# Performance work log

Hardware: AMD Instinct MI355X
Metric: run time of the kernel (lower is better)

The kernel has to match this reference:

```python
import jax, jax.numpy as jnp
import numpy as np

N = 100000   # nodes
E = 1600000  # edges
D = 128      # input_dim == hidden_dim
L = 3        # num_layers
G = 256      # graphs in batch
EPS = 1e-5   # BatchNorm eps


def setup_inputs() -> dict:
    key = jax.random.key(0)
    ks = jax.random.split(key, 10)
    x = jax.random.normal(ks[0], (N, D), dtype=jnp.float32)
    edge_index = jax.random.randint(ks[1], (2, E), 0, N, dtype=jnp.int64)
    batch = jnp.sort(jax.random.randint(ks[2], (N,), 0, G, dtype=jnp.int64))
    # stacked per-layer params (all layers are D->D since input_dim==hidden_dim)
    W = jax.random.normal(ks[3], (L, D, D), dtype=jnp.float32) * 0.05
    b = jax.random.normal(ks[4], (L, D), dtype=jnp.float32) * 0.02
    gamma = 1.0 + 0.1 * jax.random.normal(ks[5], (L, D), dtype=jnp.float32)
    beta = 0.1 * jax.random.normal(ks[6], (L, D), dtype=jnp.float32)
    rmean = 0.05 * jax.random.normal(ks[7], (L, D), dtype=jnp.float32)
    rvar = jax.random.uniform(ks[8], (L, D), minval=0.5, maxval=1.5, dtype=jnp.float32)
    return {"x": x, "W": W, "b": b, "gamma": gamma, "beta": beta,
            "rmean": rmean, "rvar": rvar, "edge_index": edge_index, "batch": batch}


def reference(x, W, b, gamma, beta, rmean, rvar, edge_index, batch):
    # --- GCN normalization with self-loops (same for every layer) ---
    src, dst = edge_index[0], edge_index[1]
    loop = jnp.arange(N, dtype=src.dtype)
    s = jnp.concatenate([src, loop])  # [E+N]
    d = jnp.concatenate([dst, loop])
    deg = jax.ops.segment_sum(jnp.ones(E + N, x.dtype), d, num_segments=N)
    dinv = jnp.where(deg > 0, jax.lax.rsqrt(deg), 0.0)
    norm = dinv[s] * dinv[d]  # [E+N]

    h = x
    for i in range(L):
        m = h @ W[i]                                            # [N, D] dense GEMM
        agg = jax.ops.segment_sum(m[s] * norm[:, None], d, num_segments=N)
        h = agg + b[i]
        # BatchNorm1d (inference: running stats), then ReLU; dropout is identity in eval
        h = (h - rmean[i]) * jax.lax.rsqrt(rvar[i] + EPS) * gamma[i] + beta[i]
        h = jax.nn.relu(h)

    # --- global mean / max pooling by graph id ---
    counts = jax.ops.segment_sum(jnp.ones(N, h.dtype), batch, num_segments=G)
    mean_pool = jax.ops.segment_sum(h, batch, num_segments=G) / jnp.maximum(counts, 1.0)[:, None]
    max_pool = jax.ops.segment_max(h, batch, num_segments=G)
    return jnp.concatenate([mean_pool, max_pool], axis=1)  # [G, 2D]
```

## Files before the change

kernel.cpp:

```cpp
#include <hip/hip_runtime.h>
#include <math.h>
#include <float.h>

#define D 128

typedef short short8 __attribute__((ext_vector_type(8)));
typedef float f32x4 __attribute__((ext_vector_type(4)));

__device__ __forceinline__ unsigned int bf16r(float f) {
    unsigned int u = __float_as_uint(f);
    return (u + 0x7fffu + ((u >> 16) & 1u)) >> 16;
}
__device__ __forceinline__ float bf2f(unsigned int lo16) {
    return __uint_as_float(lo16 << 16);
}

#define GBM0 64
__global__ __launch_bounds__(256) void prep_fused(
    const int* __restrict__ dst, int* __restrict__ cnt, int* __restrict__ rank, int E,
    const float* __restrict__ x, unsigned short* __restrict__ mraw, int n,
    const float* __restrict__ W, const float* __restrict__ b,
    const float* __restrict__ gamma, const float* __restrict__ beta,
    const float* __restrict__ rmean, const float* __restrict__ rvar,
    unsigned short* __restrict__ Wt, float* __restrict__ sc, float* __restrict__ sh, int L_,
    const int* __restrict__ batch, int* __restrict__ gstart, int G,
    int cb, int gb, int wb) {
    __shared__ short Wl[D * 136];
    const int blk = blockIdx.x;
    const int tid = threadIdx.x;
    if (blk < cb) {
        int base = (blk * 256 + tid) * 4;
        if (base + 4 <= E) {
            int4 d = *(const int4*)&dst[base];
            int r0 = atomicAdd(&cnt[d.x], 1);
            int r1 = atomicAdd(&cnt[d.y], 1);
            int r2 = atomicAdd(&cnt[d.z], 1);
            int r3 = atomicAdd(&cnt[d.w], 1);
            *(int4*)&rank[base] = make_int4(r0, r1, r2, r3);
        } else if (base < E) {
            for (int e = base; e < E; ++e) rank[e] = atomicAdd(&cnt[dst[e]], 1);
        }
    } else if (blk < cb + gb) {
#pragma unroll
        for (int i = 0; i < 64; ++i) {
            int t = i * 256 + tid;
            int k = t >> 7, r = t & 127;
            Wl[r * 136 + k] = (short)bf16r(W[t]);
        }
        __syncthreads();

        const int row0 = (blk - cb) * GBM0;
        const int wid = tid >> 6;
        const int lane = tid & 63;
        const int lr = lane & 15;
        const int lg = lane >> 4;
        const int grow = row0 + wid * 16 + lr;
        const bool valid = grow < n;

        f32x4 acc[8];
#pragma unroll
        for (int fc = 0; fc < 8; ++fc) acc[fc] = (f32x4){0.f, 0.f, 0.f, 0.f};

#pragma unroll
        for (int ks = 0; ks < 4; ++ks) {
            int kb = ks * 32 + lg * 8;
            float4 va = make_float4(0.f, 0.f, 0.f, 0.f);
            float4 vb = make_float4(0.f, 0.f, 0.f, 0.f);
            if (valid) {
                va = *(const float4*)&x[(size_t)grow * D + kb];
                vb = *(const float4*)&x[(size_t)grow * D + kb + 4];
            }
            uint4 pk;
            pk.x = bf16r(va.x) | (bf16r(va.y) << 16);
            pk.y = bf16r(va.z) | (bf16r(va.w) << 16);
            pk.z = bf16r(vb.x) | (bf16r(vb.y) << 16);
            pk.w = bf16r(vb.z) | (bf16r(vb.w) << 16);
            short8 y = *(short8*)&pk;
#pragma unroll
            for (int fc = 0; fc < 8; ++fc) {
                short8 xf = *(const short8*)&Wl[(fc * 16 + lr) * 136 + kb];
                acc[fc] = __builtin_amdgcn_mfma_f32_16x16x32_bf16(xf, y, acc[fc], 0, 0, 0);
            }
        }

        if (valid) {
#pragma unroll
            for (int fc = 0; fc < 8; ++fc) {
                int gcol = fc * 16 + lg * 4;
                uint2 pk;
                pk.x = bf16r(acc[fc][0]) | (bf16r(acc[fc][1]) << 16);
                pk.y = bf16r(acc[fc][2]) | (bf16r(acc[fc][3]) << 16);
                *(uint2*)&mraw[(size_t)grow * D + gcol] = pk;
            }
        }
    } else if (blk < cb + gb + wb) {
        int t = (blk - cb - gb) * 256 + tid;
        int total = L_ * D * D;
        if (t < total) {
            int l = t / (D * D), rem = t % (D * D);
            int r = rem >> 7, k = rem & 127;
            Wt[t] = (unsigned short)bf16r(W[l * D * D + k * D + r]);
        }
        if (t < L_ * D) {
            float inv = rsqrtf(rvar[t] + 1e-5f);
            float s = inv * gamma[t];
            sc[t] = s;
            sh[t] = (b[t] - rmean[t]) * s + beta[t];
        }
    } else {
        int i = (blk - cb - gb - wb) * 256 + tid;
        if (i >= n) return;
        int g = batch[i];
        int gp = (i == 0) ? -1 : batch[i - 1];
        for (int gg = gp + 1; gg <= g; ++gg) gstart[gg] = i;
        if (i == n - 1) for (int gg = g + 1; gg <= G; ++gg) gstart[gg] = n;
    }
}


__global__ void scan1(const int* __restrict__ cnt, int* __restrict__ rp, int* __restrict__ aux,
                      float* __restrict__ dinv, int n) {
    __shared__ int sh[256];
    int tid = threadIdx.x;
    int base = blockIdx.x * 1024 + tid * 4;
    int v[4]; int s = 0;
#pragma unroll
    for (int i = 0; i < 4; i++) {
        int idx = base + i;
        int t = (idx < n) ? cnt[idx] : 0;
        if (idx < n) dinv[idx] = rsqrtf((float)t + 1.0f);
        v[i] = s; s += t;
    }
    sh[tid] = s; __syncthreads();
    for (int off = 1; off < 256; off <<= 1) {
        int t = (tid >= off) ? sh[tid - off] : 0;
        __syncthreads();
        sh[tid] += t;
        __syncthreads();
    }
    int excl = sh[tid] - s;
#pragma unroll
    for (int i = 0; i < 4; i++) { int idx = base + i; if (idx < n) rp[idx] = excl + v[i]; }
    if (tid == 255) aux[blockIdx.x] = sh[255];
}

__global__ void scan2(int* aux, int nb) {
    __shared__ int sh[256];
    int tid = threadIdx.x;
    int v = (tid < nb) ? aux[tid] : 0;
    sh[tid] = v; __syncthreads();
    for (int off = 1; off < 256; off <<= 1) {
        int t = (tid >= off) ? sh[tid - off] : 0;
        __syncthreads();
        sh[tid] += t;
        __syncthreads();
    }
    if (tid < nb) aux[tid] = sh[tid] - v;
}

__global__ __launch_bounds__(256) void fill_scale(
    const int* __restrict__ src, const int* __restrict__ dst,
    const int* __restrict__ rp, const int* __restrict__ aux,
    const int* __restrict__ rank, int* __restrict__ csr, int E,
    unsigned int* __restrict__ M, const float* __restrict__ dinv, int n,
    int fb) {
    const int blk = blockIdx.x;
    const int tid = threadIdx.x;
    if (blk < fb) {
        int base = (blk * 256 + tid) * 4;
        if (base + 4 <= E) {
            int4 d = *(const int4*)&dst[base];
            int4 s = *(const int4*)&src[base];
            int4 r = *(const int4*)&rank[base];
            int p0 = rp[d.x] + aux[d.x >> 10];
            int p1 = rp[d.y] + aux[d.y >> 10];
            int p2 = rp[d.z] + aux[d.z >> 10];
            int p3 = rp[d.w] + aux[d.w >> 10];
            csr[p0 + r.x] = s.x;
            csr[p1 + r.y] = s.y;
            csr[p2 + r.z] = s.z;
            csr[p3 + r.w] = s.w;
        } else if (base < E) {
            for (int e = base; e < E; ++e)
                csr[rp[dst[e]] + aux[dst[e] >> 10] + rank[e]] = src[e];
        }
    } else {
        int t = (blk - fb) * 256 + tid;
        int total4 = n * 16;
        if (t >= total4) return;
        int row = t >> 4;
        float di = dinv[row];
        uint4 v = *(uint4*)&M[(size_t)t * 4];
        uint4 o;
        o.x = bf16r(bf2f(v.x & 0xffffu) * di) | (bf16r(bf2f(v.x >> 16) * di) << 16);
        o.y = bf16r(bf2f(v.y & 0xffffu) * di) | (bf16r(bf2f(v.y >> 16) * di) << 16);
        o.z = bf16r(bf2f(v.z & 0xffffu) * di) | (bf16r(bf2f(v.z >> 16) * di) << 16);
        o.w = bf16r(bf2f(v.w & 0xffffu) * di) | (bf16r(bf2f(v.w >> 16) * di) << 16);
        *(uint4*)&M[(size_t)t * 4] = o;
    }
}

#define GBM 128
__global__ __launch_bounds__(512) void gemm_mfma(const unsigned short* __restrict__ hin,
                                                 const unsigned short* __restrict__ Wt,
                                                 const float* __restrict__ dinv,
                                                 unsigned short* __restrict__ mout, int n) {
    __shared__ short Ah[GBM * 136];
    __shared__ short Wl[D * 136];
    const int tid = threadIdx.x;
    const int row0 = blockIdx.x * GBM;

#pragma unroll
    for (int i = 0; i < 4; ++i) {
        int c = tid + i * 512;
        int r = c >> 4, ck = (c & 15) * 8;
        int grow = row0 + r;
        int4 v = make_int4(0, 0, 0, 0);
        if (grow < n) v = *(const int4*)&hin[(size_t)grow * D + ck];
        *(int4*)&Ah[r * 136 + ck] = v;
    }
#pragma unroll
    for (int i = 0; i < 4; ++i) {
        int c = tid + i * 512;
        int r = c >> 4, ck = (c & 15) * 8;
        *(int4*)&Wl[r * 136 + ck] = *(const int4*)&Wt[(size_t)r * D + ck];
    }
    __syncthreads();

    const int wid = tid >> 6;
    const int lane = tid & 63;
    const int lr = lane & 15;
    const int lg = lane >> 4;

    f32x4 acc[8];
#pragma unroll
    for (int fc = 0; fc < 8; ++fc) acc[fc] = (f32x4){0.f, 0.f, 0.f, 0.f};

#pragma unroll
    for (int ks = 0; ks < 4; ++ks) {
        int kb = ks * 32 + lg * 8;
        short8 y = *(const short8*)&Ah[(wid * 16 + lr) * 136 + kb];
#pragma unroll
        for (int fc = 0; fc < 8; ++fc) {
            short8 xf = *(const short8*)&Wl[(fc * 16 + lr) * 136 + kb];
            acc[fc] = __builtin_amdgcn_mfma_f32_16x16x32_bf16(xf, y, acc[fc], 0, 0, 0);
        }
    }

    int grow = row0 + wid * 16 + lr;
    if (grow < n) {
        float di = dinv[grow];
#pragma unroll
        for (int fc = 0; fc < 8; ++fc) {
            int gcol = fc * 16 + lg * 4;
            uint2 pk;
            pk.x = bf16r(acc[fc][0] * di) | (bf16r(acc[fc][1] * di) << 16);
            pk.y = bf16r(acc[fc][2] * di) | (bf16r(acc[fc][3] * di) << 16);
            *(uint2*)&mout[(size_t)grow * D + gcol] = pk;
        }
    }
}

__global__ __launch_bounds__(256) void agg_bf16(const unsigned int* __restrict__ M,
                                                const int* __restrict__ rp,
                                                const int* __restrict__ aux,
                                                const int* __restrict__ csr,
                                                const float* __restrict__ dinv,
                                                const float* __restrict__ sc,
                                                const float* __restrict__ sh,
                                                unsigned int* __restrict__ H, int n, int Etot) {
    const int wid = threadIdx.x >> 6;
    const int lane = threadIdx.x & 63;
    const int row = blockIdx.x * 4 + wid;
    if (row >= n) return;

    unsigned int u = M[(unsigned)row * 64u + lane];
    float a0 = bf2f(u & 0xffffu);
    float a1 = bf2f(u >> 16);

    int e = rp[row] + aux[row >> 10];
    const int end = (row + 1 < n) ? rp[row + 1] + aux[(row + 1) >> 10] : Etot;
    const int n16 = (end - e) >> 4;

    if (n16 > 0) {
        int sa[16];
#pragma unroll
        for (int i = 0; i < 16; ++i) sa[i] = csr[e + i];
        for (int it = 0; it < n16; ++it) {
            int sb[16];
            if (it + 1 < n16) {
#pragma unroll
                for (int i = 0; i < 16; ++i) sb[i] = csr[e + 16 + i];
            } else {
#pragma unroll
                for (int i = 0; i < 16; ++i) sb[i] = 0;
            }
            unsigned int g[16];
#pragma unroll
            for (int i = 0; i < 16; ++i) g[i] = M[(unsigned)sa[i] * 64u + lane];
#pragma unroll
            for (int i = 0; i < 16; ++i) {
                a0 += bf2f(g[i] & 0xffffu);
                a1 += bf2f(g[i] >> 16);
            }
#pragma unroll
            for (int i = 0; i < 16; ++i) sa[i] = sb[i];
            e += 16;
        }
    }
    for (; e + 4 <= end; e += 4) {
        int s[4];
#pragma unroll
        for (int i = 0; i < 4; ++i) s[i] = csr[e + i];
        unsigned int g[4];
#pragma unroll
        for (int i = 0; i < 4; ++i) g[i] = M[(unsigned)s[i] * 64u + lane];
#pragma unroll
        for (int i = 0; i < 4; ++i) {
            a0 += bf2f(g[i] & 0xffffu);
            a1 += bf2f(g[i] >> 16);
        }
    }
    for (; e < end; ++e) {
        unsigned int gs = M[(unsigned)csr[e] * 64u + lane];
        a0 += bf2f(gs & 0xffffu);
        a1 += bf2f(gs >> 16);
    }

    float di = dinv[row];
    int c0 = lane * 2;
    float v0 = fmaxf(a0 * di * sc[c0] + sh[c0], 0.f);
    float v1 = fmaxf(a1 * di * sc[c0 + 1] + sh[c0 + 1], 0.f);
    H[(unsigned)row * 64u + lane] = bf16r(v0) | (bf16r(v1) << 16);
}

__global__ __launch_bounds__(64) void pool1(const unsigned int* __restrict__ H,
                                            const int* __restrict__ gstart,
                                            float4* __restrict__ pbuf) {
    int g = blockIdx.x, c = blockIdx.y;
    int lane = threadIdx.x;
    int beg = gstart[g], end = gstart[g + 1];
    int len = end - beg;
    int cb = beg + (int)(((long long)len * c) >> 3);
    int ce = beg + (int)(((long long)len * (c + 1)) >> 3);
    float s0 = 0.f, s1 = 0.f, m0 = -INFINITY, m1 = -INFINITY;
    int i = cb;
    for (; i + 2 <= ce; i += 2) {
        unsigned int ua = H[(size_t)i * 64 + lane];
        unsigned int ub = H[(size_t)(i + 1) * 64 + lane];
        float a0 = bf2f(ua & 0xffffu), a1 = bf2f(ua >> 16);
        float b0 = bf2f(ub & 0xffffu), b1 = bf2f(ub >> 16);
        s0 += a0 + b0; s1 += a1 + b1;
        m0 = fmaxf(m0, fmaxf(a0, b0)); m1 = fmaxf(m1, fmaxf(a1, b1));
    }
    for (; i < ce; ++i) {
        unsigned int ua = H[(size_t)i * 64 + lane];
        float a0 = bf2f(ua & 0xffffu), a1 = bf2f(ua >> 16);
        s0 += a0; s1 += a1;
        m0 = fmaxf(m0, a0); m1 = fmaxf(m1, a1);
    }
    pbuf[((size_t)g * 8 + c) * 64 + lane] = make_float4(s0, s1, m0, m1);
}

__global__ __launch_bounds__(64) void pool2(const float4* __restrict__ pbuf,
                                            const int* __restrict__ gstart,
                                            float* __restrict__ out) {
    int g = blockIdx.x;
    int lane = threadIdx.x;
    float s0 = 0.f, s1 = 0.f, m0 = -INFINITY, m1 = -INFINITY;
#pragma unroll
    for (int c = 0; c < 8; ++c) {
        float4 p = pbuf[((size_t)g * 8 + c) * 64 + lane];
        s0 += p.x; s1 += p.y;
        m0 = fmaxf(m0, p.z); m1 = fmaxf(m1, p.w);
    }
    float cnt = fmaxf((float)(gstart[g + 1] - gstart[g]), 1.0f);
    int c0 = lane * 2;
    out[g * (2 * D) + c0] = s0 / cnt;
    out[g * (2 * D) + c0 + 1] = s1 / cnt;
    out[g * (2 * D) + D + c0] = m0;
    out[g * (2 * D) + D + c0 + 1] = m1;
}

extern "C" void kernel_launch(void* const* d_in, const int* in_sizes, int n_in,
                              void* d_out, int out_size, void* d_ws, size_t ws_size,
                              hipStream_t stream) {
    const float* x     = (const float*)d_in[0];
    const float* W     = (const float*)d_in[1];
    const float* b     = (const float*)d_in[2];
    const float* gamma = (const float*)d_in[3];
    const float* beta  = (const float*)d_in[4];
    const float* rmean = (const float*)d_in[5];
    const float* rvar  = (const float*)d_in[6];
    const int*   eidx  = (const int*)d_in[7];
    const int*   batch = (const int*)d_in[8];

    const int N = in_sizes[8];
    const int E = in_sizes[7] / 2;
    const int L = in_sizes[2] / D;
    const int G = out_size / (2 * D);

    const int* esrc = eidx;
    const int* edst = eidx + E;

    size_t off = 0;
    auto carve = [&](size_t bytes) { size_t cur = off; off += (bytes + 255) & ~(size_t)255; return cur; };
    char* base = (char*)d_ws;
    const int nb = (N + 1023) / 1024;

    int*            cnt  = (int*)           (base + carve((size_t)N * 4));
    int*            rp   = (int*)           (base + carve((size_t)(N + 1) * 4));
    int*            aux  = (int*)           (base + carve((size_t)nb * 4));
    float*          dinv = (float*)         (base + carve((size_t)N * 4));
    int*            rank = (int*)           (base + carve((size_t)E * 4));
    int*            csr  = (int*)           (base + carve((size_t)E * 4));
    unsigned short* hbuf = (unsigned short*)(base + carve((size_t)N * D * 2));
    unsigned short* mbuf = (unsigned short*)(base + carve((size_t)N * D * 2));
    unsigned short* Wt   = (unsigned short*)(base + carve((size_t)L * D * D * 2));
    float*          sc   = (float*)         (base + carve((size_t)L * D * 4));
    float*          shb  = (float*)         (base + carve((size_t)L * D * 4));
    int*            gst  = (int*)           (base + carve((size_t)(G + 1) * 4));
    float4*         pbuf = (float4*)        (base + carve((size_t)G * 8 * 64 * 16));
    (void)ws_size;

    hipMemsetAsync(cnt, 0, (size_t)N * 4, stream);

    const int cb = ((E + 3) / 4 + 255) / 256;
    const int gb = (N + GBM0 - 1) / GBM0;
    const int wb = (L * D * D + 255) / 256;
    const int bb = (N + 255) / 256;
    const int gemmb = (N + GBM - 1) / GBM;
    const int fb = ((E + 3) / 4 + 255) / 256;
    const int sb = (N * 16 + 255) / 256;
    const int aggb = (N + 3) / 4;

    prep_fused<<<cb + gb + wb + bb, 256, 0, stream>>>(edst, cnt, rank, E,
                                                      x, mbuf, N,
                                                      W, b, gamma, beta, rmean, rvar,
                                                      Wt, sc, shb, L,
                                                      batch, gst, G, cb, gb, wb);
    scan1<<<nb, 256, 0, stream>>>(cnt, rp, aux, dinv, N);
    scan2<<<1, 256, 0, stream>>>(aux, nb);

    fill_scale<<<fb + sb, 256, 0, stream>>>(esrc, edst, rp, aux, rank, csr, E,
                                            (unsigned int*)mbuf, dinv, N, fb);

    agg_bf16<<<aggb, 256, 0, stream>>>((const unsigned int*)mbuf, rp, aux, csr, dinv,
                                       sc, shb, (unsigned int*)hbuf, N, E);

    for (int l = 1; l < L; ++l) {
        gemm_mfma<<<gemmb, 512, 0, stream>>>(hbuf, Wt + (size_t)l * D * D, dinv, mbuf, N);
        agg_bf16<<<aggb, 256, 0, stream>>>((const unsigned int*)mbuf, rp, aux, csr, dinv,
                                           sc + l * D, shb + l * D,
                                           (unsigned int*)hbuf, N, E);
    }

    pool1<<<dim3(G, 8), 64, 0, stream>>>((const unsigned int*)hbuf, gst, pbuf);
    pool2<<<G, 64, 0, stream>>>(pbuf, gst, (float*)d_out);
}
```

Before: 375.6 us.

## Move layer-0 GEMM after degree scan and fold dinv scaling into its epilogue

The first-layer GEMM moves out of the prep kernel into a new kernel that runs after the degree scan. That lets it multiply by dinv in its epilogue and write pre-scaled bf16 rows directly. This removes the separate read-modify-write pass over the N×D message buffer that the fill_scale kernel performed. The CSR fill blocks now share a launch with the GEMM using 512-thread blocks. The GEMM no longer overlaps with the atomic counting phase, and it now loads the pre-transposed bf16 weights instead of converting W itself.

```diff
diff --git a/kernel.cpp b/kernel.cpp
--- a/kernel.cpp
+++ b/kernel.cpp
@@ -15,19 +15,16 @@
     return __uint_as_float(lo16 << 16);
 }
 
-#define GBM0 64
 __global__ __launch_bounds__(256) void prep_fused(
     const int* __restrict__ dst, int* __restrict__ cnt, int* __restrict__ rank, int E,
-    const float* __restrict__ x, unsigned short* __restrict__ mraw, int n,
     const float* __restrict__ W, const float* __restrict__ b,
     const float* __restrict__ gamma, const float* __restrict__ beta,
     const float* __restrict__ rmean, const float* __restrict__ rvar,
     unsigned short* __restrict__ Wt, float* __restrict__ sc, float* __restrict__ sh, int L_,
-    const int* __restrict__ batch, int* __restrict__ gstart, int G,
-    int cb, int gb, int wb) {
-    __shared__ short Wl[D * 136];
-    const int blk = blockIdx.x;
-    const int tid = threadIdx.x;
+    const int* __restrict__ batch, int* __restrict__ gstart, int n, int G,
+    int cb, int wb) {
+    int blk = blockIdx.x;
+    int tid = threadIdx.x;
     if (blk < cb) {
         int base = (blk * 256 + tid) * 4;
         if (base + 4 <= E) {
@@ -40,61 +37,8 @@
         } else if (base < E) {
             for (int e = base; e < E; ++e) rank[e] = atomicAdd(&cnt[dst[e]], 1);
         }
-    } else if (blk < cb + gb) {
-#pragma unroll
-        for (int i = 0; i < 64; ++i) {
-            int t = i * 256 + tid;
-            int k = t >> 7, r = t & 127;
-            Wl[r * 136 + k] = (short)bf16r(W[t]);
-        }
-        __syncthreads();
-
-        const int row0 = (blk - cb) * GBM0;
-        const int wid = tid >> 6;
-        const int lane = tid & 63;
-        const int lr = lane & 15;
-        const int lg = lane >> 4;
-        const int grow = row0 + wid * 16 + lr;
-        const bool valid = grow < n;
-
-        f32x4 acc[8];
-#pragma unroll
-        for (int fc = 0; fc < 8; ++fc) acc[fc] = (f32x4){0.f, 0.f, 0.f, 0.f};
-
-#pragma unroll
-        for (int ks = 0; ks < 4; ++ks) {
-            int kb = ks * 32 + lg * 8;
-            float4 va = make_float4(0.f, 0.f, 0.f, 0.f);
-            float4 vb = make_float4(0.f, 0.f, 0.f, 0.f);
-            if (valid) {
-                va = *(const float4*)&x[(size_t)grow * D + kb];
-                vb = *(const float4*)&x[(size_t)grow * D + kb + 4];
-            }
-            uint4 pk;
-            pk.x = bf16r(va.x) | (bf16r(va.y) << 16);
-            pk.y = bf16r(va.z) | (bf16r(va.w) << 16);
-            pk.z = bf16r(vb.x) | (bf16r(vb.y) << 16);
-            pk.w = bf16r(vb.z) | (bf16r(vb.w) << 16);
-            short8 y = *(short8*)&pk;
-#pragma unroll
-            for (int fc = 0; fc < 8; ++fc) {
-                short8 xf = *(const short8*)&Wl[(fc * 16 + lr) * 136 + kb];
-                acc[fc] = __builtin_amdgcn_mfma_f32_16x16x32_bf16(xf, y, acc[fc], 0, 0, 0);
-            }
-        }
-
-        if (valid) {
-#pragma unroll
-            for (int fc = 0; fc < 8; ++fc) {
-                int gcol = fc * 16 + lg * 4;
-                uint2 pk;
-                pk.x = bf16r(acc[fc][0]) | (bf16r(acc[fc][1]) << 16);
-                pk.y = bf16r(acc[fc][2]) | (bf16r(acc[fc][3]) << 16);
-                *(uint2*)&mraw[(size_t)grow * D + gcol] = pk;
-            }
-        }
-    } else if (blk < cb + gb + wb) {
-        int t = (blk - cb - gb) * 256 + tid;
+    } else if (blk < cb + wb) {
+        int t = (blk - cb) * 256 + tid;
         int total = L_ * D * D;
         if (t < total) {
             int l = t / (D * D), rem = t % (D * D);
@@ -108,7 +52,7 @@
             sh[t] = (b[t] - rmean[t]) * s + beta[t];
         }
     } else {
-        int i = (blk - cb - gb - wb) * 256 + tid;
+        int i = (blk - cb - wb) * 256 + tid;
         if (i >= n) return;
         int g = batch[i];
         int gp = (i == 0) ? -1 : batch[i - 1];
@@ -158,16 +102,81 @@
     if (tid < nb) aux[tid] = sh[tid] - v;
 }
 
-__global__ __launch_bounds__(256) void fill_scale(
+#define GBM 128
+__device__ __forceinline__ void gemm0_body(short* Wl, const float* __restrict__ x,
+                                           const unsigned short* __restrict__ Wt,
+                                           const float* __restrict__ dinv,
+                                           unsigned short* __restrict__ mout, int n, int blk) {
+    const int tid = threadIdx.x;
+    const int row0 = blk * GBM;
+
+#pragma unroll
+    for (int i = 0; i < 4; ++i) {
+        int c = tid + i * 512;
+        int r = c >> 4, ck = (c & 15) * 8;
+        *(int4*)&Wl[r * 136 + ck] = *(const int4*)&Wt[(size_t)r * D + ck];
+    }
+    __syncthreads();
+
+    const int wid = tid >> 6;
+    const int lane = tid & 63;
+    const int lr = lane & 15;
+    const int lg = lane >> 4;
+
+    const int grow = row0 + wid * 16 + lr;
+    const bool valid = grow < n;
+
+    f32x4 acc[8];
+#pragma unroll
+    for (int fc = 0; fc < 8; ++fc) acc[fc] = (f32x4){0.f, 0.f, 0.f, 0.f};
+
+#pragma unroll
+    for (int ks = 0; ks < 4; ++ks) {
+        int kb = ks * 32 + lg * 8;
+        float4 va = make_float4(0.f, 0.f, 0.f, 0.f);
+        float4 vb = make_float4(0.f, 0.f, 0.f, 0.f);
+        if (valid) {
+            va = *(const float4*)&x[(size_t)grow * D + kb];
+            vb = *(const float4*)&x[(size_t)grow * D + kb + 4];
+        }
+        uint4 pk;
+        pk.x = bf16r(va.x) | (bf16r(va.y) << 16);
+        pk.y = bf16r(va.z) | (bf16r(va.w) << 16);
+        pk.z = bf16r(vb.x) | (bf16r(vb.y) << 16);
+        pk.w = bf16r(vb.z) | (bf16r(vb.w) << 16);
+        short8 y = *(short8*)&pk;
+#pragma unroll
+        for (int fc = 0; fc < 8; ++fc) {
+            short8 xf = *(const short8*)&Wl[(fc * 16 + lr) * 136 + kb];
+            acc[fc] = __builtin_amdgcn_mfma_f32_16x16x32_bf16(xf, y, acc[fc], 0, 0, 0);
+        }
+    }
+
+    if (valid) {
+        float di = dinv[grow];
+#pragma unroll
+        for (int fc = 0; fc < 8; ++fc) {
+            int gcol = fc * 16 + lg * 4;
+            uint2 pk;
+            pk.x = bf16r(acc[fc][0] * di) | (bf16r(acc[fc][1] * di) << 16);
+            pk.y = bf16r(acc[fc][2] * di) | (bf16r(acc[fc][3] * di) << 16);
+            *(uint2*)&mout[(size_t)grow * D + gcol] = pk;
+        }
+    }
+}
+
+__global__ __launch_bounds__(512) void fused_fill_gemm0(
+    const float* __restrict__ x, const unsigned short* __restrict__ Wt,
+    const float* __restrict__ dinv, unsigned short* __restrict__ mout, int n,
     const int* __restrict__ src, const int* __restrict__ dst,
     const int* __restrict__ rp, const int* __restrict__ aux,
-    const int* __restrict__ rank, int* __restrict__ csr, int E,
-    unsigned int* __restrict__ M, const float* __restrict__ dinv, int n,
-    int fb) {
-    const int blk = blockIdx.x;
-    const int tid = threadIdx.x;
-    if (blk < fb) {
-        int base = (blk * 256 + tid) * 4;
+    const int* __restrict__ rank, int* __restrict__ csr, int E, int gemmb) {
+    __shared__ short Wl[D * 136];
+    if ((int)blockIdx.x < gemmb) {
+        gemm0_body(Wl, x, Wt, dinv, mout, n, blockIdx.x);
+    } else {
+        int gblk = blockIdx.x - gemmb;
+        int base = (gblk * 512 + (int)threadIdx.x) * 4;
         if (base + 4 <= E) {
             int4 d = *(const int4*)&dst[base];
             int4 s = *(const int4*)&src[base];
@@ -184,23 +193,9 @@
             for (int e = base; e < E; ++e)
                 csr[rp[dst[e]] + aux[dst[e] >> 10] + rank[e]] = src[e];
         }
-    } else {
-        int t = (blk - fb) * 256 + tid;
-        int total4 = n * 16;
-        if (t >= total4) return;
-        int row = t >> 4;
-        float di = dinv[row];
-        uint4 v = *(uint4*)&M[(size_t)t * 4];
-        uint4 o;
-        o.x = bf16r(bf2f(v.x & 0xffffu) * di) | (bf16r(bf2f(v.x >> 16) * di) << 16);
-        o.y = bf16r(bf2f(v.y & 0xffffu) * di) | (bf16r(bf2f(v.y >> 16) * di) << 16);
-        o.z = bf16r(bf2f(v.z & 0xffffu) * di) | (bf16r(bf2f(v.z >> 16) * di) << 16);
-        o.w = bf16r(bf2f(v.w & 0xffffu) * di) | (bf16r(bf2f(v.w >> 16) * di) << 16);
-        *(uint4*)&M[(size_t)t * 4] = o;
-    }
-}
-
-#define GBM 128
+    }
+}
+
 __global__ __launch_bounds__(512) void gemm_mfma(const unsigned short* __restrict__ hin,
                                                  const unsigned short* __restrict__ Wt,
                                                  const float* __restrict__ dinv,
@@ -426,25 +421,21 @@
     hipMemsetAsync(cnt, 0, (size_t)N * 4, stream);
 
     const int cb = ((E + 3) / 4 + 255) / 256;
-    const int gb = (N + GBM0 - 1) / GBM0;
     const int wb = (L * D * D + 255) / 256;
     const int bb = (N + 255) / 256;
     const int gemmb = (N + GBM - 1) / GBM;
-    const int fb = ((E + 3) / 4 + 255) / 256;
-    const int sb = (N * 16 + 255) / 256;
+    const int fb = ((E + 3) / 4 + 511) / 512;
     const int aggb = (N + 3) / 4;
 
-    prep_fused<<<cb + gb + wb + bb, 256, 0, stream>>>(edst, cnt, rank, E,
-                                                      x, mbuf, N,
-                                                      W, b, gamma, beta, rmean, rvar,
-                                                      Wt, sc, shb, L,
-                                                      batch, gst, G, cb, gb, wb);
+    prep_fused<<<cb + wb + bb, 256, 0, stream>>>(edst, cnt, rank, E,
+                                                 W, b, gamma, beta, rmean, rvar,
+                                                 Wt, sc, shb, L,
+                                                 batch, gst, N, G, cb, wb);
     scan1<<<nb, 256, 0, stream>>>(cnt, rp, aux, dinv, N);
     scan2<<<1, 256, 0, stream>>>(aux, nb);
 
-    fill_scale<<<fb + sb, 256, 0, stream>>>(esrc, edst, rp, aux, rank, csr, E,
-                                            (unsigned int*)mbuf, dinv, N, fb);
-
+    fused_fill_gemm0<<<gemmb + fb, 512, 0, stream>>>(x, Wt, dinv, mbuf, N,
+                                                     esrc, edst, rp, aux, rank, csr, E, gemmb);
     agg_bf16<<<aggb, 256, 0, stream>>>((const unsigned int*)mbuf, rp, aux, csr, dinv,
                                        sc, shb, (unsigned int*)hbuf, N, E);
 
```

New measurement: 367.1 us. 2.3% less time.
